# Kernel optimization log

Hardware: AMD Instinct MI355X
Metric: run time of the kernel (lower is better)

## Reference

```python
import jax, jax.numpy as jnp
import numpy as np

B, T, D_IN, H1, H2 = 32, 2048, 1024, 512, 32


def setup_inputs() -> dict:
    key = jax.random.key(0)
    ks = jax.random.split(key, 8)
    avf_out = jax.random.normal(ks[0], (B, T, D_IN), dtype=jnp.float32)
    # seq_len in [1, T] so every sample has a non-empty slice (matches torch usage)
    seq_len = jax.random.randint(ks[1], (B,), 1, T + 1, dtype=jnp.int32)
    s = 0.02
    W1 = jax.random.normal(ks[2], (D_IN, H1), dtype=jnp.float32) * s
    b1 = jnp.zeros((H1,), dtype=jnp.float32)
    W2 = jax.random.normal(ks[3], (H1, H2), dtype=jnp.float32) * s
    b2 = jnp.zeros((H2,), dtype=jnp.float32)
    W3 = jax.random.normal(ks[4], (H2, 1), dtype=jnp.float32) * s
    b3 = jnp.zeros((1,), dtype=jnp.float32)
    return {"avf_out": avf_out, "W1": W1, "b1": b1, "W2": W2, "b2": b2,
            "W3": W3, "b3": b3, "seq_len": seq_len}


def reference(avf_out, W1, b1, W2, b2, W3, b3, seq_len):
    h = jax.nn.relu(jnp.einsum('btd,dh->bth', avf_out, W1) + b1)
    h = jnp.einsum('bth,hk->btk', h, W2) + b2
    logits = jax.nn.sigmoid(jnp.einsum('btk,ko->bto', h, W3) + b3)[..., 0]  # [B, T]
    # ragged per-sample top-k (k = seq_len//16 + 1 over first seq_len entries) + mean,
    # vectorized via masked descending sort + cumsum (no per-sample loop)
    Tn = logits.shape[1]
    valid = jnp.arange(Tn)[None, :] < seq_len[:, None]            # [B, T]
    NEG = jnp.float32(-1.0)  # below sigmoid range, so padded slots never enter top-k
    masked = jnp.where(valid, logits, NEG)
    sorted_desc = -jnp.sort(-masked, axis=1)                      # [B, T] descending
    csum = jnp.cumsum(sorted_desc, axis=1)
    k = seq_len // 16 + 1                                         # k <= seq_len always
    topk_sum = jnp.take_along_axis(csum, (k - 1)[:, None].astype(jnp.int32), axis=1)[:, 0]
    return topk_sum / k.astype(logits.dtype)                      # [B]
```

## Files before the change

kernel.cpp:

```cpp
#include <hip/hip_runtime.h>

typedef __bf16 bf16;
typedef __bf16 bf16x4 __attribute__((ext_vector_type(4)));
typedef __bf16 bf16x8 __attribute__((ext_vector_type(8)));
typedef float f32x4 __attribute__((ext_vector_type(4)));

#define K_TOT 1024
#define N_TOT 512
#define T_SEQ 2048
#define NB 32
#define M_TILE 160
#define MAX_J 13
#define ROW_MAX (NB * T_SEQ - 1)

__device__ __forceinline__ void async16(const void* g, void* l) {
    __builtin_amdgcn_global_load_lds(
        (const __attribute__((address_space(1))) unsigned int*)g,
        (__attribute__((address_space(3))) unsigned int*)l, 16, 0, 0);
}

__global__ __launch_bounds__(256) void transpose_prep(
        const float* __restrict__ W1, bf16* __restrict__ W1T,
        const float* __restrict__ W2, const float* __restrict__ b2,
        const float* __restrict__ W3, const float* __restrict__ b3,
        const int* __restrict__ seq_len,
        float* __restrict__ v, int* __restrict__ tiles, int* __restrict__ done) {
    __shared__ float tile[32][33];
    __shared__ int nb2[32], off2[32];
    const int t = threadIdx.x;
    const int k0 = blockIdx.x * 32;
    const int n0 = blockIdx.y * 32;
#pragma unroll
    for (int p = 0; p < 4; p++) {
        int kl = p * 8 + (t >> 5);
        int nl = t & 31;
        tile[kl][nl] = W1[(k0 + kl) * 512 + n0 + nl];
    }
    __syncthreads();
#pragma unroll
    for (int p = 0; p < 4; p++) {
        int nl = p * 8 + (t >> 5);
        int kl = t & 31;
        W1T[(n0 + nl) * 1024 + k0 + kl] = (bf16)tile[kl][nl];
    }

    if (blockIdx.x == 0 && blockIdx.y == 0) {
        for (int h = t; h < 512; h += 256) {
            float s = 0.f;
#pragma unroll
            for (int c = 0; c < 32; c++) s += W2[h * 32 + c] * W3[c];
            v[h] = s;
        }
        if (t == 0) {
            float cc = b3[0];
            for (int c = 0; c < 32; c++) cc += b2[c] * W3[c];
            v[512] = cc;
        }
        if (t < 32) {
            nb2[t] = (seq_len[t] + M_TILE - 1) / M_TILE;
            done[t] = 0;
        }
        __syncthreads();
        if (t == 0) {
            int a = 0;
            for (int i = 0; i < 32; i++) { off2[i] = a; a += nb2[i]; }
            tiles[0] = a;
        }
        __syncthreads();
        for (int idx = t; idx < 512; idx += 256) {
            int b = idx >> 4, j = idx & 15;
            if (j < nb2[b]) tiles[1 + off2[b] + j] = (b << 4) | j;
        }
    }
}

__device__ __forceinline__ int sw_idx(int row, int e) {
    return row * 64 + (((e >> 3) ^ (row & 7)) << 3) + (e & 7);
}

__global__ __launch_bounds__(512, 2) void gemm_fused(const float* __restrict__ A,
                                                     const bf16* __restrict__ W1T,
                                                     const float* __restrict__ b1,
                                                     const float* __restrict__ v,
                                                     const int* __restrict__ tiles,
                                                     const int* __restrict__ seq_len,
                                                     int* __restrict__ done,
                                                     float* __restrict__ logits,
                                                     float* __restrict__ out) {
    __shared__ bf16 smem[M_TILE * 64 + 2 * N_TOT * 64];
    bf16* As = smem;
    bf16* Bs0 = smem + M_TILE * 64;
    bf16* Bs1 = Bs0 + N_TOT * 64;

    const int nact = tiles[0];
    if ((int)blockIdx.x >= nact) return;
    const int tileid = tiles[1 + blockIdx.x];
    const int bsmp = tileid >> 4;
    const int jj = tileid & 15;
    const int m0 = bsmp * T_SEQ + jj * M_TILE;

    const int t = threadIdx.x;
    const int wave = t >> 6, lane = t & 63;
    const int q = lane >> 4, l15 = lane & 15;
    const int wm = wave >> 2, wn = wave & 3;

    const int c16 = t & 15, r0 = t >> 4;
    const float* agp[5];
#pragma unroll
    for (int p = 0; p < 5; p++) {
        int grow = m0 + r0 + p * 32;
        if (grow > ROW_MAX) grow = ROW_MAX;
        agp[p] = A + (size_t)grow * K_TOT + c16 * 4;
    }

    const int bl_row = wave * 64 + (lane >> 3);
    const int bl_chunk = (lane & 7) ^ ((lane >> 3) & 7);
    const bf16* bgp = W1T + (size_t)bl_row * K_TOT + bl_chunk * 8;

    f32x4 acc[5][8] = {};
    float4 av[5];

    auto loadA = [&](int k0) {
#pragma unroll
        for (int p = 0; p < 5; p++) av[p] = *(const float4*)(agp[p] + k0);
    };
    auto asyncB = [&](int k0, bf16* bs) {
#pragma unroll
        for (int j = 0; j < 8; j++)
            async16(bgp + k0 + (size_t)j * 8 * K_TOT, bs + (wave * 64 + j * 8) * 64);
    };
    auto writeA = [&]() {
#pragma unroll
        for (int p = 0; p < 5; p++) {
            bf16x4 w;
            w[0] = (bf16)av[p].x; w[1] = (bf16)av[p].y;
            w[2] = (bf16)av[p].z; w[3] = (bf16)av[p].w;
            int row = r0 + p * 32;
            int chunk = c16 >> 1;
            int idx = row * 64 + ((chunk ^ (row & 7)) << 3) + (c16 & 1) * 4;
            *(bf16x4*)(&As[idx]) = w;
        }
    };
    auto mfma_phase = [&](const bf16* bs) {
#pragma unroll
        for (int kk = 0; kk < 64; kk += 32) {
            const int e = kk + q * 8;
            bf16x8 af[5];
#pragma unroll
            for (int mi = 0; mi < 5; mi++)
                af[mi] = *(const bf16x8*)(&As[sw_idx(wm * 80 + mi * 16 + l15, e)]);
#pragma unroll
            for (int nh = 0; nh < 8; nh += 4) {
                bf16x8 bfv[4];
#pragma unroll
                for (int ni = 0; ni < 4; ni++)
                    bfv[ni] = *(const bf16x8*)(&bs[sw_idx(wn * 128 + (nh + ni) * 16 + l15, e)]);
#pragma unroll
                for (int mi = 0; mi < 5; mi++)
#pragma unroll
                    for (int ni = 0; ni < 4; ni++)
                        acc[mi][nh + ni] = __builtin_amdgcn_mfma_f32_16x16x32_bf16(
                            af[mi], bfv[ni], acc[mi][nh + ni], 0, 0, 0);
            }
        }
    };

    loadA(0);
    asyncB(0, Bs0);
    writeA();
    __syncthreads();

#pragma unroll 1
    for (int k = 0; k < 16; k++) {
        bf16* bcur = (k & 1) ? Bs1 : Bs0;
        bf16* bnxt = (k & 1) ? Bs0 : Bs1;
        if (k < 15) {
            loadA((k + 1) * 64);
            asyncB((k + 1) * 64, bnxt);
        }
        mfma_phase(bcur);
        __syncthreads();
        if (k < 15) {
            writeA();
            __syncthreads();
        }
    }

    float bb[8], vv[8];
#pragma unroll
    for (int ni = 0; ni < 8; ni++) {
        int col = wn * 128 + ni * 16 + l15;
        bb[ni] = b1[col];
        vv[ni] = v[col];
    }
    const float cconst = v[512];

    float* part = (float*)smem;

#pragma unroll
    for (int mi = 0; mi < 5; mi++) {
#pragma unroll
        for (int r = 0; r < 4; r++) {
            float s = 0.f;
#pragma unroll
            for (int ni = 0; ni < 8; ni++)
                s += fmaxf(acc[mi][ni][r] + bb[ni], 0.f) * vv[ni];
            s += __shfl_xor(s, 1);
            s += __shfl_xor(s, 2);
            s += __shfl_xor(s, 4);
            s += __shfl_xor(s, 8);
            if (l15 == 0) {
                int row = wm * 80 + mi * 16 + q * 4 + r;
                part[row * 4 + wn] = s;
            }
        }
    }
    __syncthreads();
    if (t < M_TILE && jj * M_TILE + t < T_SEQ) {
        float s = part[t * 4] + part[t * 4 + 1] + part[t * 4 + 2] + part[t * 4 + 3] + cconst;
        logits[m0 + t] = 1.f / (1.f + __expf(-s));
    }

    const int L = seq_len[bsmp];
    const int nb = (L + M_TILE - 1) / M_TILE;

    float* vals  = (float*)smem;
    int*   redi  = (int*)(vals + 2048);
    unsigned* mnx = (unsigned*)(redi + 16);
    float* redf  = (float*)(mnx + 16);
    int*   wflag = (int*)(redf + 8);

    __syncthreads();
    if (t == 0) {
        __threadfence();
        int old = atomicAdd(&done[bsmp], 1);
        int win = (old == nb - 1);
        if (win) __threadfence();
        *wflag = win;
    }
    __syncthreads();
    if (!*wflag) return;

    const int kk = (L >> 4) + 1;
    const float* p = logits + bsmp * T_SEQ;

    unsigned mn = 0x3f800000u, mx = 0u;
    for (int i = t; i < L; i += 512) {
        float x = p[i];
        vals[i] = x;
        unsigned u = __float_as_uint(x);
        mn = min(mn, u); mx = max(mx, u);
    }
#pragma unroll
    for (int m = 32; m >= 1; m >>= 1) {
        mn = min(mn, (unsigned)__shfl_xor((int)mn, m));
        mx = max(mx, (unsigned)__shfl_xor((int)mx, m));
    }
    if (lane == 0) { mnx[wave] = mn; mnx[8 + wave] = mx; }
    __syncthreads();
    unsigned lo = mnx[0], hi = mnx[8];
#pragma unroll
    for (int w8 = 1; w8 < 8; w8++) {
        lo = min(lo, mnx[w8]); hi = max(hi, mnx[8 + w8]);
    }
    __syncthreads();

    int rb = 0;
    while (lo < hi) {
        unsigned w = hi - lo;
        unsigned t1 = w / 3u + 1u;
        unsigned m1 = lo + t1;
        unsigned m2 = lo + (w - w / 3u);
        if (m2 < m1) m2 = m1;
        float f1 = __uint_as_float(m1), f2 = __uint_as_float(m2);
        int c1 = 0, c2 = 0;
        for (int i = t; i < L; i += 512) {
            float x = vals[i];
            c1 += (x >= f1) ? 1 : 0;
            c2 += (x >= f2) ? 1 : 0;
        }
        int packed = (c1 << 12) | c2;
#pragma unroll
        for (int m = 32; m >= 1; m >>= 1) packed += __shfl_xor(packed, m);
        if (lane == 0) redi[(rb & 1) * 8 + wave] = packed;
        __syncthreads();
        int tot = 0;
#pragma unroll
        for (int w8 = 0; w8 < 8; w8++) tot += redi[(rb & 1) * 8 + w8];
        int C2 = tot & 0xFFF, C1 = tot >> 12;
        if (C2 >= kk)      { lo = m2; }
        else if (C1 >= kk) { lo = m1; hi = m2 - 1; }
        else               { hi = m1 - 1; }
        rb++;
    }
    const float thr = __uint_as_float(lo);

    int cg = 0; float sg = 0.f;
    for (int i = t; i < L; i += 512) {
        float x = vals[i];
        if (x > thr) { cg += 1; sg += x; }
    }
#pragma unroll
    for (int m = 32; m >= 1; m >>= 1) {
        cg += __shfl_xor(cg, m);
        sg += __shfl_xor(sg, m);
    }
    if (lane == 0) { redi[(rb & 1) * 8 + wave] = cg; redf[wave] = sg; }
    __syncthreads();
    if (t == 0) {
        int cgt = 0; float sgt = 0.f;
#pragma unroll
        for (int w8 = 0; w8 < 8; w8++) { cgt += redi[(rb & 1) * 8 + w8]; sgt += redf[w8]; }
        out[bsmp] = (sgt + (float)(kk - cgt) * thr) / (float)kk;
    }
}

extern "C" void kernel_launch(void* const* d_in, const int* in_sizes, int n_in,
                              void* d_out, int out_size, void* d_ws, size_t ws_size,
                              hipStream_t stream) {
    const float* avf = (const float*)d_in[0];
    const float* W1  = (const float*)d_in[1];
    const float* b1  = (const float*)d_in[2];
    const float* W2  = (const float*)d_in[3];
    const float* b2  = (const float*)d_in[4];
    const float* W3  = (const float*)d_in[5];
    const float* b3  = (const float*)d_in[6];
    const int* seq_len = (const int*)d_in[7];
    float* out = (float*)d_out;

    char* ws = (char*)d_ws;
    bf16*  W1T    = (bf16*)ws;
    float* v      = (float*)(ws + (1 << 20));
    int*   tiles  = (int*)(ws + (1 << 20) + 4096);
    int*   done   = (int*)(ws + (1 << 20) + 8192);
    float* logits = (float*)(ws + (1 << 20) + 12288);

    transpose_prep<<<dim3(32, 16), 256, 0, stream>>>(W1, W1T, W2, b2, W3, b3,
                                                     seq_len, v, tiles, done);
    gemm_fused<<<NB * MAX_J, 512, 0, stream>>>(avf, W1T, b1, v, tiles, seq_len,
                                               done, logits, out);
}
```

Baseline: 397.6 us.

## Rebalance GEMM tiles into evenly sized per-sample chunks targeting full CU occupancy

Instead of fixed 160-row tiles per sample, the prep kernel splits each sample's valid rows into near-equal chunks, adding chunks greedily to the longest ones until about 256 blocks exist. The GEMM kernel decodes start/row-count per tile, skips loading rows beyond its count, and the completion counter tracks rows rather than tiles. This aims to reduce tail imbalance and fill all CUs, at the cost of each block still computing full 160-row MFMA tiles and re-reading W1 more often.

```diff
diff --git a/kernel.cpp b/kernel.cpp
--- a/kernel.cpp
+++ b/kernel.cpp
@@ -11,7 +11,7 @@
 #define NB 32
 #define M_TILE 160
 #define MAX_J 13
-#define ROW_MAX (NB * T_SEQ - 1)
+#define NBLK_TGT 256
 
 __device__ __forceinline__ void async16(const void* g, void* l) {
     __builtin_amdgcn_global_load_lds(
@@ -26,7 +26,7 @@
         const int* __restrict__ seq_len,
         float* __restrict__ v, int* __restrict__ tiles, int* __restrict__ done) {
     __shared__ float tile[32][33];
-    __shared__ int nb2[32], off2[32];
+    __shared__ int nb2[32], off2[32], Ls[32];
     const int t = threadIdx.x;
     const int k0 = blockIdx.x * 32;
     const int n0 = blockIdx.y * 32;
@@ -57,19 +57,39 @@
             v[512] = cc;
         }
         if (t < 32) {
-            nb2[t] = (seq_len[t] + M_TILE - 1) / M_TILE;
+            int L = seq_len[t];
+            Ls[t] = L;
+            nb2[t] = (L + M_TILE - 1) / M_TILE;
             done[t] = 0;
         }
         __syncthreads();
         if (t == 0) {
+            int tot = 0;
+            for (int i = 0; i < 32; i++) tot += nb2[i];
+            while (tot < NBLK_TGT) {
+                int best = -1, bestr = 1;
+                for (int i = 0; i < 32; i++) {
+                    int r = (Ls[i] + nb2[i] - 1) / nb2[i];
+                    if (r > bestr && nb2[i] < Ls[i]) { bestr = r; best = i; }
+                }
+                if (best < 0) break;
+                nb2[best]++; tot++;
+            }
             int a = 0;
             for (int i = 0; i < 32; i++) { off2[i] = a; a += nb2[i]; }
             tiles[0] = a;
         }
         __syncthreads();
-        for (int idx = t; idx < 512; idx += 256) {
-            int b = idx >> 4, j = idx & 15;
-            if (j < nb2[b]) tiles[1 + off2[b] + j] = (b << 4) | j;
+        for (int idx = t; idx < 32 * 256; idx += 256) {
+            int b = idx >> 8, j = idx & 255;
+            int nb = nb2[b];
+            if (j < nb) {
+                int L = Ls[b];
+                int q = L / nb, r = L % nb;
+                int start = j * q + (j < r ? j : r);
+                int nrows = q + (j < r ? 1 : 0);
+                tiles[1 + off2[b] + j] = (b << 19) | (start << 8) | nrows;
+            }
         }
     }
 }
@@ -94,10 +114,11 @@
 
     const int nact = tiles[0];
     if ((int)blockIdx.x >= nact) return;
-    const int tileid = tiles[1 + blockIdx.x];
-    const int bsmp = tileid >> 4;
-    const int jj = tileid & 15;
-    const int m0 = bsmp * T_SEQ + jj * M_TILE;
+    const int w = tiles[1 + blockIdx.x];
+    const int bsmp = w >> 19;
+    const int start = (w >> 8) & 0x7FF;
+    const int mrows = w & 0xFF;
+    const int m0 = bsmp * T_SEQ + start;
 
     const int t = threadIdx.x;
     const int wave = t >> 6, lane = t & 63;
@@ -107,11 +128,8 @@
     const int c16 = t & 15, r0 = t >> 4;
     const float* agp[5];
 #pragma unroll
-    for (int p = 0; p < 5; p++) {
-        int grow = m0 + r0 + p * 32;
-        if (grow > ROW_MAX) grow = ROW_MAX;
-        agp[p] = A + (size_t)grow * K_TOT + c16 * 4;
-    }
+    for (int p = 0; p < 5; p++)
+        agp[p] = A + (size_t)(m0 + r0 + p * 32) * K_TOT + c16 * 4;
 
     const int bl_row = wave * 64 + (lane >> 3);
     const int bl_chunk = (lane & 7) ^ ((lane >> 3) & 7);
@@ -122,7 +140,8 @@
 
     auto loadA = [&](int k0) {
 #pragma unroll
-        for (int p = 0; p < 5; p++) av[p] = *(const float4*)(agp[p] + k0);
+        for (int p = 0; p < 5; p++)
+            if (r0 + p * 32 < mrows) av[p] = *(const float4*)(agp[p] + k0);
     };
     auto asyncB = [&](int k0, bf16* bs) {
 #pragma unroll
@@ -132,13 +151,14 @@
     auto writeA = [&]() {
 #pragma unroll
         for (int p = 0; p < 5; p++) {
-            bf16x4 w;
-            w[0] = (bf16)av[p].x; w[1] = (bf16)av[p].y;
-            w[2] = (bf16)av[p].z; w[3] = (bf16)av[p].w;
+            if (r0 + p * 32 >= mrows) continue;
+            bf16x4 wv;
+            wv[0] = (bf16)av[p].x; wv[1] = (bf16)av[p].y;
+            wv[2] = (bf16)av[p].z; wv[3] = (bf16)av[p].w;
             int row = r0 + p * 32;
             int chunk = c16 >> 1;
             int idx = row * 64 + ((chunk ^ (row & 7)) << 3) + (c16 & 1) * 4;
-            *(bf16x4*)(&As[idx]) = w;
+            *(bf16x4*)(&As[idx]) = wv;
         }
     };
     auto mfma_phase = [&](const bf16* bs) {
@@ -216,13 +236,12 @@
         }
     }
     __syncthreads();
-    if (t < M_TILE && jj * M_TILE + t < T_SEQ) {
+    if (t < mrows) {
         float s = part[t * 4] + part[t * 4 + 1] + part[t * 4 + 2] + part[t * 4 + 3] + cconst;
         logits[m0 + t] = 1.f / (1.f + __expf(-s));
     }
 
     const int L = seq_len[bsmp];
-    const int nb = (L + M_TILE - 1) / M_TILE;
 
     float* vals  = (float*)smem;
     int*   redi  = (int*)(vals + 2048);
@@ -233,8 +252,8 @@
     __syncthreads();
     if (t == 0) {
         __threadfence();
-        int old = atomicAdd(&done[bsmp], 1);
-        int win = (old == nb - 1);
+        int old = atomicAdd(&done[bsmp], mrows);
+        int win = (old + mrows == L);
         if (win) __threadfence();
         *wflag = win;
     }
@@ -267,10 +286,10 @@
 
     int rb = 0;
     while (lo < hi) {
-        unsigned w = hi - lo;
-        unsigned t1 = w / 3u + 1u;
+        unsigned wd = hi - lo;
+        unsigned t1 = wd / 3u + 1u;
         unsigned m1 = lo + t1;
-        unsigned m2 = lo + (w - w / 3u);
+        unsigned m2 = lo + (wd - wd / 3u);
         if (m2 < m1) m2 = m1;
         float f1 = __uint_as_float(m1), f2 = __uint_as_float(m2);
         int c1 = 0, c2 = 0;
```

Measured after the change: 460.7 us. +15.9%, slower.
